# Kernel tuning notes

Measured on AMD Instinct MI355X. Metric: run time of the kernel, lower is better.

## Reference

```python
import jax, jax.numpy as jnp
import numpy as np

K = 3
OFFSET_SCALE = 0.25
GN_GROUPS = 8
GN_EPS = 1e-5


def setup_inputs() -> dict:
    key = jax.random.key(0)
    k1, k2, k3 = jax.random.split(key, 3)
    N, C, H, W = 4, 128, 96, 96
    Cout = 128
    x = jax.random.normal(k1, (N, C, H, W), dtype=jnp.float32)
    # offset head: small random weights so offsets are modest (tanh tames anyway)
    w_head = jax.random.normal(k2, (3, C, 3, 3), dtype=jnp.float32) * 0.05
    b_head = jnp.zeros((3,), dtype=jnp.float32)
    # kaiming-ish scale for the deform conv weight: sqrt(2 / fan_out)
    w_dcn = jax.random.normal(k3, (Cout, C, 3, 3), dtype=jnp.float32) * np.sqrt(2.0 / (Cout * 9))
    gn_gamma = jnp.ones((Cout,), dtype=jnp.float32)
    gn_beta = jnp.zeros((Cout,), dtype=jnp.float32)
    return {"x": x, "w_head": w_head, "b_head": b_head, "w_dcn": w_dcn,
            "gn_gamma": gn_gamma, "gn_beta": gn_beta}


def _conv3x3(x, w, b):
    y = jax.lax.conv_general_dilated(
        x, w, window_strides=(1, 1), padding=((1, 1), (1, 1)),
        dimension_numbers=("NCHW", "OIHW", "NCHW"))
    return y + b[None, :, None, None]


def _deform_sample(xn, py, px):
    # xn: (C,H,W); py/px: (9,H,W) absolute sampling coords (y=row, x=col)
    C, H, W = xn.shape
    y0 = jnp.floor(py).astype(jnp.int32)
    x0 = jnp.floor(px).astype(jnp.int32)
    fy = py - y0
    fx = px - x0
    xf = xn.reshape(C, H * W)

    def corner(yi, xi, wgt):
        valid = (yi >= 0) & (yi < H) & (xi >= 0) & (xi < W)
        idx = jnp.clip(yi, 0, H - 1) * W + jnp.clip(xi, 0, W - 1)  # (9,H,W)
        v = xf[:, idx.reshape(-1)].reshape(C, *idx.shape)  # (C,9,H,W)
        return v * (wgt * valid)[None]

    return (corner(y0, x0, (1 - fy) * (1 - fx))
            + corner(y0, x0 + 1, (1 - fy) * fx)
            + corner(y0 + 1, x0, fy * (1 - fx))
            + corner(y0 + 1, x0 + 1, fy * fx))


def reference(x, w_head, b_head, w_dcn, gn_gamma, gn_beta):
    N, C, H, W = x.shape
    Cout = w_dcn.shape[0]
    stride, pad, dil = 1, 1, 1

    head = _conv3x3(x, w_head, b_head)                 # (N,3,H,W)
    dx, dy, m = head[:, :1], head[:, 1:2], head[:, 2:3]
    mask = jax.nn.sigmoid(m)                           # (N,1,H,W) broadcast over 9 taps
    dx = OFFSET_SCALE * jnp.tanh(dx)
    dy = OFFSET_SCALE * jnp.tanh(dy)

    # serpentine 18-channel offsets, mmcv layout: (oy, ox) pairs per kernel tap
    z = jnp.zeros_like(dx)
    offs = jnp.concatenate(
        [z, z, z, dy, z, -dy, dx, z, z, z, -dx, z, dx, dy, dx, -dy, -dx, dy], axis=1)
    offs = offs.reshape(N, 9, 2, H, W)
    oy, ox = offs[:, :, 0], offs[:, :, 1]              # (N,9,H,W)

    ky = jnp.arange(9) // 3
    kx = jnp.arange(9) % 3
    base_y = (jnp.arange(H) * stride - pad)[None, :, None] + (ky * dil)[:, None, None]
    base_x = (jnp.arange(W) * stride - pad)[None, None, :] + (kx * dil)[:, None, None]
    py = base_y[None] + oy                             # (N,9,H,W)
    px = base_x[None] + ox

    sampled = jax.vmap(_deform_sample)(x, py, px)      # (N,C,9,H,W)
    sampled = sampled * mask[:, None]                  # modulated

    y = jnp.einsum('nckhw,ock->nohw', sampled, w_dcn.reshape(Cout, C, 9))

    # GroupNorm(8, Cout) + ReLU
    G = min(GN_GROUPS, Cout)
    yg = y.reshape(N, G, Cout // G, H, W)
    mu = yg.mean(axis=(2, 3, 4), keepdims=True)
    var = yg.var(axis=(2, 3, 4), keepdims=True)
    yn = ((yg - mu) * jax.lax.rsqrt(var + GN_EPS)).reshape(N, Cout, H, W)
    yn = yn * gn_gamma[None, :, None, None] + gn_beta[None, :, None, None]
    return jax.nn.relu(yn)
```

## Files before the change

### kernel.cpp

```cpp
#include <hip/hip_runtime.h>
#include <hip/hip_bf16.h>
#include <math.h>

#define NB   4
#define CIN  128
#define HH   96
#define WW   96
#define HWN  (HH*WW)
#define NHW  (NB*HWN)
#define COUT 128
#define KW   9
#define KDIM (CIN*KW)
#define GSZ  16
#define PXB  32
#define NBLK (NHW/PXB)

typedef __attribute__((ext_vector_type(8))) short bf16x8;
typedef __attribute__((ext_vector_type(4))) float f32x4;

#define OFF_WAH   0
#define OFF_DX    147456
#define OFF_DY    184320
#define OFF_MASK  221184
#define OFF_GN    258048
#define OFF_MAP   258240
#define OFF_PAIR  258496

#define HEADB 1152

__device__ __forceinline__ ushort f2bf(float f) {
    union { float f; uint u; } v; v.f = f;
    uint r = v.u + 0x7fffu + ((v.u >> 16) & 1u);
    return (ushort)(r >> 16);
}
__device__ __forceinline__ float bf2f(ushort h) {
    union { uint u; float f; } v; v.u = ((uint)h) << 16;
    return v.f;
}

__device__ __forceinline__ void barrier_keep_vm() {
    asm volatile("s_waitcnt lgkmcnt(0)\n\ts_barrier" ::: "memory");
}

__global__ __launch_bounds__(256) void pre_kernel(const float* __restrict__ x,
                                                  const float* __restrict__ w_head,
                                                  const float* __restrict__ b_head,
                                                  const float* __restrict__ wd,
                                                  ushort* __restrict__ wah,
                                                  float* __restrict__ dxv,
                                                  float* __restrict__ dyv,
                                                  float* __restrict__ maskv,
                                                  float* __restrict__ gn_part,
                                                  int* __restrict__ map,
                                                  int* __restrict__ pairB) {
    __shared__ float wl[CIN * 28];
    __shared__ float sp[32][8][13];
    const int b = blockIdx.x, t = threadIdx.x;

    if (b >= HEADB) {
        const int bb = b - HEADB;
        int i = bb * 256 + t;
        {
            int e  = i & 7;
            int l  = (i >> 3) & 63;
            int ot = (i >> 9) & 7;
            int q  = (i >> 12) & 3;
            int k  = i >> 14;
            int o  = ot * 16 + (l & 15);
            int c  = q * 32 + (l >> 4) * 8 + e;
            wah[i] = f2bf(wd[o * KDIM + c * KW + k]);
        }
        if (bb == 0 && t < 128) gn_part[t] = 0.f;
        if (bb == 0 && t < 64) {
            int l = t;
            bf16x8 A1 = {}, B1 = {}, A2 = {}, B2 = {};
            if ((l >> 4) == 0) {
                A1[0] = (short)f2bf((float)((l & 15) + 1));
                B1[0] = (short)f2bf(1.0f);
                A2[0] = (short)f2bf(1.0f);
                B2[0] = (short)f2bf((float)((l & 15) + 1));
            }
            f32x4 d1 = {0.f,0.f,0.f,0.f}, d2 = {0.f,0.f,0.f,0.f};
            d1 = __builtin_amdgcn_mfma_f32_16x16x32_bf16(A1, B1, d1, 0, 0, 0);
            d2 = __builtin_amdgcn_mfma_f32_16x16x32_bf16(A2, B2, d2, 0, 0, 0);
#pragma unroll
            for (int r = 0; r < 4; ++r) {
                int m = (int)(d1[r] + 0.5f) - 1;
                int n = (int)(d2[r] + 0.5f) - 1;
                map[l * 4 + r] = (m << 4) | n;
            }
        }
        if (bb == 1 && t < 64) {
            int l = t;
            union { bf16x8 v; short a[8]; } B;
#pragma unroll
            for (int e = 0; e < 8; ++e) {
                float val = (float)(1u << (((l >> 4) * 8 + e) & 31));
                B.a[e] = (short)f2bf(val);
            }
#pragma unroll
            for (int s = 0; s < 32; ++s) {
                union { bf16x8 v; short a[8]; } A;
#pragma unroll
                for (int e = 0; e < 8; ++e) A.a[e] = 0;
                if ((l >> 4) == (s >> 3)) A.a[s & 7] = (short)f2bf(1.0f);
                f32x4 d = {0.f, 0.f, 0.f, 0.f};
                d = __builtin_amdgcn_mfma_f32_16x16x32_bf16(A.v, B.v, d, 0, 0, 0);
                float v0 = d[0];
                if (l == 0 && v0 > 0.f) {
                    int ex; frexpf(v0, &ex);
                    int j = ex - 1;
                    if (j >= 0 && j < 32) pairB[j] = s;
                }
            }
        }
        return;
    }

    for (int i = t; i < 3456; i += 256) {
        int j = i / KDIM, r = i - j * KDIM;
        int c = r / 9, kk = r - c * 9;
        wl[c * 28 + kk * 3 + j] = w_head[i];
    }
    __syncthreads();

    const int sl = t & 7;
    const int cg = t >> 3;
    const int p0 = b * 32 + sl * 4;
    const int n  = p0 / HWN;
    const int hw = p0 - n * HWN;
    const int h  = hw / WW;
    const int w0 = hw - h * WW;
    const float* xn = x + (size_t)n * CIN * HWN;
    const bool lok = (w0 > 0);
    const bool rok = (w0 < WW - 4);

    float acc[12];
#pragma unroll
    for (int i = 0; i < 12; ++i) acc[i] = 0.f;

#pragma unroll
    for (int cc = 0; cc < 4; ++cc) {
        const int c = cg * 4 + cc;
        const float* xc = xn + (size_t)c * HWN;
        float v[3][6];
#pragma unroll
        for (int r = 0; r < 3; ++r) {
            int y = h - 1 + r;
            if (y >= 0 && y < HH) {
                const float* xr = xc + y * WW + w0;
                float4 m4 = *(const float4*)xr;
                v[r][1] = m4.x; v[r][2] = m4.y; v[r][3] = m4.z; v[r][4] = m4.w;
                v[r][0] = lok ? xr[-1] : 0.f;
                v[r][5] = rok ? xr[4]  : 0.f;
            } else {
#pragma unroll
                for (int i = 0; i < 6; ++i) v[r][i] = 0.f;
            }
        }
        float wr[28];
        const float* wc = &wl[c * 28];
#pragma unroll
        for (int i2 = 0; i2 < 7; ++i2) {
            float4 q4 = *(const float4*)(wc + i2 * 4);
            wr[i2 * 4 + 0] = q4.x; wr[i2 * 4 + 1] = q4.y;
            wr[i2 * 4 + 2] = q4.z; wr[i2 * 4 + 3] = q4.w;
        }
#pragma unroll
        for (int ky = 0; ky < 3; ++ky)
#pragma unroll
            for (int kx = 0; kx < 3; ++kx) {
                const int kk = ky * 3 + kx;
                const float wj0 = wr[kk * 3 + 0];
                const float wj1 = wr[kk * 3 + 1];
                const float wj2 = wr[kk * 3 + 2];
#pragma unroll
                for (int q = 0; q < 4; ++q) {
                    float val = v[ky][q + kx];
                    acc[q * 3 + 0] = fmaf(val, wj0, acc[q * 3 + 0]);
                    acc[q * 3 + 1] = fmaf(val, wj1, acc[q * 3 + 1]);
                    acc[q * 3 + 2] = fmaf(val, wj2, acc[q * 3 + 2]);
                }
            }
    }
#pragma unroll
    for (int i = 0; i < 12; ++i) sp[cg][sl][i] = acc[i];
    __syncthreads();
    if (cg < 8) {
#pragma unroll
        for (int k = 8; k < 32; k += 8)
#pragma unroll
            for (int i = 0; i < 12; ++i) sp[cg][sl][i] += sp[cg + k][sl][i];
    }
    __syncthreads();
    if (t < 32) {
        const int s2 = t >> 2, q = t & 3;
        float b0 = b_head[0], b1 = b_head[1], b2 = b_head[2];
#pragma unroll
        for (int cgi = 0; cgi < 8; ++cgi) {
            b0 += sp[cgi][s2][q * 3 + 0];
            b1 += sp[cgi][s2][q * 3 + 1];
            b2 += sp[cgi][s2][q * 3 + 2];
        }
        int pp = b * 32 + t;
        dxv[pp]   = 0.25f * tanhf(b0);
        dyv[pp]   = 0.25f * tanhf(b1);
        maskv[pp] = 1.f / (1.f + expf(-b2));
    }
}

__global__ __launch_bounds__(256) void dcn_kernel(const float* __restrict__ x,
                                                  const ushort* __restrict__ wah,
                                                  const float* __restrict__ dxv,
                                                  const float* __restrict__ dyv,
                                                  const float* __restrict__ maskv,
                                                  const int* __restrict__ map,
                                                  const int* __restrict__ pairB,
                                                  float* __restrict__ out,
                                                  float* __restrict__ gn_part) {
    __shared__ __attribute__((aligned(16))) ushort sBh[2][4 * PXB * 8];
    __shared__ float sMask[PXB];
    __shared__ float gred[16];

    const int t = threadIdx.x;
    const int lane = t & 63;
    const int wv = t >> 6;
    const int lg = lane >> 4;
    const int ml = lane & 15;
    const int pix = t & 31;
    const int sg  = t >> 5;

    int b = blockIdx.x;
    int nb = (b & 7) * (NBLK / 8) + (b >> 3);
    const int p0  = nb * PXB;
    const int n   = p0 / HWN;
    const int hw0 = p0 % HWN;
    const float* xn = x + (size_t)n * CIN * HWN;

    if (t < PXB) sMask[t] = maskv[p0 + t];
    if (t < 16) gred[t] = 0.f;

    const float dxl = dxv[p0 + pix];
    const float dyl = dyv[p0 + pix];
    const int hme = (hw0 + pix) / WW;
    const int wme = (hw0 + pix) % WW;

    int chn[4];
#pragma unroll
    for (int e = 0; e < 4; ++e) chn[e] = pairB[sg * 4 + e] & 31;

    f32x4 acc[2][2];
#pragma unroll
    for (int i = 0; i < 2; i++)
#pragma unroll
        for (int j = 0; j < 2; j++) acc[i][j] = (f32x4){0.f, 0.f, 0.f, 0.f};

    const int oyc[9] = {0, 0, 0, 1, 0, -1, 1, 1, -1};
    const int oxc[9] = {0, 1, -1, 0, 0, 0, 1, -1, 1};
    const int ncl[9] = {1, 2, 2, 2, 1, 2, 4, 4, 4};

    int aa[4]; float wq[4];
    float raw[4][4];
    bf16x8 An0, An1;

    {
        float py = (float)(hme - 1), px = (float)(wme - 1);
        float fy0 = floorf(py), fx0 = floorf(px);
        int y0 = (int)fy0, x0 = (int)fx0;
        float fy = py - fy0, fx = px - fx0;
#pragma unroll
        for (int j = 0; j < 4; ++j) {
            int yy = y0 + (j >> 1), xx = x0 + (j & 1);
            float wb = ((j >> 1) ? fy : 1.f - fy) * ((j & 1) ? fx : 1.f - fx);
            bool ok = (yy >= 0) && (yy < HH) && (xx >= 0) && (xx < WW);
            aa[j] = min(max(yy, 0), HH - 1) * WW + min(max(xx, 0), WW - 1);
            wq[j] = ok ? wb : 0.f;
        }
#pragma unroll
        for (int e = 0; e < 4; ++e) raw[e][0] = xn[(size_t)chn[e] * HWN + aa[0]];
        const size_t abase = (size_t)(wv * 2) * 512 + lane * 8;
        An0 = *(const bf16x8*)(wah + abase);
        An1 = *(const bf16x8*)(wah + abase + 512);
    }

#pragma unroll
    for (int j = 0; j < 36; ++j) {
        const int k = j >> 2;
        const int NC = ncl[k];
        bf16x8 Ah0 = An0, Ah1 = An1;
        union { short4 v; ushort u[4]; } hv;
#pragma unroll
        for (int e = 0; e < 4; ++e) {
            float s = raw[e][0] * wq[0];
            if (NC >= 2) s += raw[e][1] * wq[1];
            if (NC == 4) s += raw[e][2] * wq[2] + raw[e][3] * wq[3];
            hv.u[e] = f2bf(s);
        }
        const int wbase = ((sg >> 1) * PXB + pix) * 8 + (sg & 1) * 4;
        *(short4*)&sBh[j & 1][wbase] = hv.v;
        if (j < 35) {
            const int jn = j + 1, kn = jn >> 2, qn = jn & 3;
            if (qn == 0) {
                const int ky = kn / 3, kx = kn - ky * 3;
                float py = (float)(hme - 1 + ky) + (float)oyc[kn] * dxl;
                float px = (float)(wme - 1 + kx) + (float)oxc[kn] * dyl;
                float fy0 = floorf(py), fx0 = floorf(px);
                int y0 = (int)fy0, x0 = (int)fx0;
                float fy = py - fy0, fx = px - fx0;
#pragma unroll
                for (int jj = 0; jj < 4; ++jj) {
                    int yy = y0 + (jj >> 1), xx = x0 + (jj & 1);
                    float wb = ((jj >> 1) ? fy : 1.f - fy) * ((jj & 1) ? fx : 1.f - fx);
                    bool ok = (yy >= 0) && (yy < HH) && (xx >= 0) && (xx < WW);
                    aa[jj] = min(max(yy, 0), HH - 1) * WW + min(max(xx, 0), WW - 1);
                    wq[jj] = ok ? wb : 0.f;
                }
                if (ncl[kn] == 2 && oxc[kn] == 0) { aa[1] = aa[2]; wq[1] = wq[2]; }
            }
            const int NCn = ncl[kn];
            const int ccn = qn * 32;
#pragma unroll
            for (int e = 0; e < 4; ++e) {
                const float* xc = xn + (size_t)(ccn + chn[e]) * HWN;
                raw[e][0] = xc[aa[0]];
                if (NCn >= 2) raw[e][1] = xc[aa[1]];
                if (NCn == 4) { raw[e][2] = xc[aa[2]]; raw[e][3] = xc[aa[3]]; }
            }
            const size_t abase = (size_t)((kn * 4 + qn) * 8 + wv * 2) * 512 + lane * 8;
            An0 = *(const bf16x8*)(wah + abase);
            An1 = *(const bf16x8*)(wah + abase + 512);
        }
        barrier_keep_vm();
#pragma unroll
        for (int pt = 0; pt < 2; ++pt) {
            const int rbase = (lg * PXB + pt * 16 + ml) * 8;
            bf16x8 Bh = *(const bf16x8*)&sBh[j & 1][rbase];
            acc[0][pt] = __builtin_amdgcn_mfma_f32_16x16x32_bf16(Ah0, Bh, acc[0][pt], 0, 0, 0);
            acc[1][pt] = __builtin_amdgcn_mfma_f32_16x16x32_bf16(Ah1, Bh, acc[1][pt], 0, 0, 0);
        }
    }

    int4 mn4 = *(const int4*)&map[lane * 4];
    int mn[4] = {mn4.x, mn4.y, mn4.z, mn4.w};
    float s1g[2] = {0.f, 0.f}, s2g[2] = {0.f, 0.f};
#pragma unroll
    for (int ot = 0; ot < 2; ++ot) {
        int otile = wv * 32 + ot * 16;
#pragma unroll
        for (int pt = 0; pt < 2; ++pt) {
#pragma unroll
            for (int r = 0; r < 4; ++r) {
                int m = mn[r] >> 4, nn2 = mn[r] & 15;
                int p = pt * 16 + nn2;
                float v = acc[ot][pt][r] * sMask[p];
                s1g[ot] += v;
                s2g[ot] += v * v;
                out[((size_t)n * COUT + otile + m) * HWN + hw0 + p] = v;
            }
        }
    }
#pragma unroll
    for (int ot = 0; ot < 2; ++ot) {
        int g = wv * 2 + ot;
        atomicAdd(&gred[g * 2 + 0], s1g[ot]);
        atomicAdd(&gred[g * 2 + 1], s2g[ot]);
    }
    __syncthreads();
    if (t < 8) {
        atomicAdd(&gn_part[n * 8 + t],      gred[t * 2 + 0]);
        atomicAdd(&gn_part[64 + n * 8 + t], gred[t * 2 + 1]);
    }
}

__global__ __launch_bounds__(256) void gn_apply(float* __restrict__ out,
                                                const float* __restrict__ gn_part,
                                                const float* __restrict__ gamma,
                                                const float* __restrict__ beta) {
    int i4 = blockIdx.x * 256 + threadIdx.x;
    size_t e = (size_t)i4 * 4;
    int og = (int)(e / HWN);
    int n = og >> 7, o = og & 127;
    int s = n * 8 + (o >> 4);
    const float cnt = (float)GSZ * (float)HWN;
    float s1 = gn_part[s], s2 = gn_part[64 + s];
    float mu = s1 / cnt;
    float var = s2 / cnt - mu * mu;
    float inv = rsqrtf(var + 1e-5f);
    float ga = gamma[o] * inv;
    float be = beta[o] - mu * ga;
    float4 v = *(float4*)(out + e);
    v.x = fmaxf(fmaf(v.x, ga, be), 0.f);
    v.y = fmaxf(fmaf(v.y, ga, be), 0.f);
    v.z = fmaxf(fmaf(v.z, ga, be), 0.f);
    v.w = fmaxf(fmaf(v.w, ga, be), 0.f);
    *(float4*)(out + e) = v;
}

extern "C" void kernel_launch(void* const* d_in, const int* in_sizes, int n_in,
                              void* d_out, int out_size, void* d_ws, size_t ws_size,
                              hipStream_t stream) {
    const float* x       = (const float*)d_in[0];
    const float* w_head  = (const float*)d_in[1];
    const float* b_head  = (const float*)d_in[2];
    const float* w_dcn   = (const float*)d_in[3];
    const float* gamma   = (const float*)d_in[4];
    const float* beta    = (const float*)d_in[5];
    float* out = (float*)d_out;
    float* ws  = (float*)d_ws;

    ushort* wah    = (ushort*)(ws + OFF_WAH);
    float* dxv     = ws + OFF_DX;
    float* dyv     = ws + OFF_DY;
    float* maskv   = ws + OFF_MASK;
    float* gn_part = ws + OFF_GN;
    int*   map     = (int*)(ws + OFF_MAP);
    int*   pairB   = (int*)(ws + OFF_PAIR);

    pre_kernel<<<HEADB + 576, 256, 0, stream>>>(x, w_head, b_head, w_dcn, wah,
                                                dxv, dyv, maskv, gn_part, map, pairB);
    dcn_kernel<<<NBLK, 256, 0, stream>>>(x, wah, dxv, dyv, maskv, map, pairB, out, gn_part);
    gn_apply<<<(NB * COUT * HWN) / 4 / 256, 256, 0, stream>>>(out, gn_part, gamma, beta);
}
```

Before: 196.1 us.

## Transpose input to channel-last with permuted channels for vectorized gathers

Adds a transpose kernel that writes x in NHWC layout with channels permuted to match the MFMA pair ordering, so each deformable-sample gather reads four contiguous channels as one float4 instead of four strided scalar loads. This is meant to cut the number of uncoalesced gather transactions in the main DCN kernel. In exchange it adds an extra pass over the full input tensor, a workspace buffer and an extra launch.

Result: no change. 194.3 us (-0.9%).

```diff
diff --git a/kernel.cpp b/kernel.cpp
--- a/kernel.cpp
+++ b/kernel.cpp
@@ -14,6 +14,7 @@
 #define GSZ  16
 #define PXB  32
 #define NBLK (NHW/PXB)
+#define XPB  64
 
 typedef __attribute__((ext_vector_type(8))) short bf16x8;
 typedef __attribute__((ext_vector_type(4))) float f32x4;
@@ -25,6 +26,7 @@
 #define OFF_GN    258048
 #define OFF_MAP   258240
 #define OFF_PAIR  258496
+#define OFF_XT    258560
 
 #define HEADB 1152
 
@@ -32,10 +34,6 @@
     union { float f; uint u; } v; v.f = f;
     uint r = v.u + 0x7fffu + ((v.u >> 16) & 1u);
     return (ushort)(r >> 16);
-}
-__device__ __forceinline__ float bf2f(ushort h) {
-    union { uint u; float f; } v; v.u = ((uint)h) << 16;
-    return v.f;
 }
 
 __device__ __forceinline__ void barrier_keep_vm() {
@@ -209,13 +207,55 @@
     }
 }
 
-__global__ __launch_bounds__(256) void dcn_kernel(const float* __restrict__ x,
+__global__ __launch_bounds__(256) void xpose_kernel(const float* __restrict__ x,
+                                                    const int* __restrict__ pairB,
+                                                    float* __restrict__ xt) {
+    __shared__ float tile[CIN][XPB + 1];
+    __shared__ int sperm[CIN];
+    const int b = blockIdx.x, t = threadIdx.x;
+    const int p0 = b * XPB;
+    const int n  = p0 / HWN, hw0 = p0 % HWN;
+    const float* xn = x + (size_t)n * CIN * HWN + hw0;
+
+    if (t < CIN) {
+        int q = t >> 5, j = t & 31;
+        sperm[t] = q * 32 + (pairB[j] & 31);
+    }
+    __syncthreads();
+
+#pragma unroll
+    for (int rep = 0; rep < 4; ++rep) {
+        const int c  = rep * 32 + (t >> 3);
+        const int px = (t & 7) * 8;
+        const float* src = xn + (size_t)c * HWN + px;
+        float4 a = *(const float4*)src;
+        float4 bq = *(const float4*)(src + 4);
+        tile[c][px + 0] = a.x;  tile[c][px + 1] = a.y;
+        tile[c][px + 2] = a.z;  tile[c][px + 3] = a.w;
+        tile[c][px + 4] = bq.x; tile[c][px + 5] = bq.y;
+        tile[c][px + 6] = bq.z; tile[c][px + 7] = bq.w;
+    }
+    __syncthreads();
+
+    const int px = t >> 2, jg = t & 3;
+    float* dst = xt + ((size_t)p0 + px) * CIN + jg * 32;
+#pragma unroll
+    for (int jj = 0; jj < 32; jj += 4) {
+        float4 v;
+        v.x = tile[sperm[jg * 32 + jj + 0]][px];
+        v.y = tile[sperm[jg * 32 + jj + 1]][px];
+        v.z = tile[sperm[jg * 32 + jj + 2]][px];
+        v.w = tile[sperm[jg * 32 + jj + 3]][px];
+        *(float4*)(dst + jj) = v;
+    }
+}
+
+__global__ __launch_bounds__(256) void dcn_kernel(const float* __restrict__ xt,
                                                   const ushort* __restrict__ wah,
                                                   const float* __restrict__ dxv,
                                                   const float* __restrict__ dyv,
                                                   const float* __restrict__ maskv,
                                                   const int* __restrict__ map,
-                                                  const int* __restrict__ pairB,
                                                   float* __restrict__ out,
                                                   float* __restrict__ gn_part) {
     __shared__ __attribute__((aligned(16))) ushort sBh[2][4 * PXB * 8];
@@ -235,7 +275,7 @@
     const int p0  = nb * PXB;
     const int n   = p0 / HWN;
     const int hw0 = p0 % HWN;
-    const float* xn = x + (size_t)n * CIN * HWN;
+    const float* xtn = xt + (size_t)n * HWN * CIN;
 
     if (t < PXB) sMask[t] = maskv[p0 + t];
     if (t < 16) gred[t] = 0.f;
@@ -245,10 +285,6 @@
     const int hme = (hw0 + pix) / WW;
     const int wme = (hw0 + pix) % WW;
 
-    int chn[4];
-#pragma unroll
-    for (int e = 0; e < 4; ++e) chn[e] = pairB[sg * 4 + e] & 31;
-
     f32x4 acc[2][2];
 #pragma unroll
     for (int i = 0; i < 2; i++)
@@ -260,7 +296,7 @@
     const int ncl[9] = {1, 2, 2, 2, 1, 2, 4, 4, 4};
 
     int aa[4]; float wq[4];
-    float raw[4][4];
+    float4 vr0, vr1, vr2, vr3;
     bf16x8 An0, An1;
 
     {
@@ -276,8 +312,7 @@
             aa[j] = min(max(yy, 0), HH - 1) * WW + min(max(xx, 0), WW - 1);
             wq[j] = ok ? wb : 0.f;
         }
-#pragma unroll
-        for (int e = 0; e < 4; ++e) raw[e][0] = xn[(size_t)chn[e] * HWN + aa[0]];
+        vr0 = *(const float4*)(xtn + ((aa[0] << 7) + sg * 4));
         const size_t abase = (size_t)(wv * 2) * 512 + lane * 8;
         An0 = *(const bf16x8*)(wah + abase);
         An1 = *(const bf16x8*)(wah + abase + 512);
@@ -289,12 +324,21 @@
         const int NC = ncl[k];
         bf16x8 Ah0 = An0, Ah1 = An1;
         union { short4 v; ushort u[4]; } hv;
-#pragma unroll
-        for (int e = 0; e < 4; ++e) {
-            float s = raw[e][0] * wq[0];
-            if (NC >= 2) s += raw[e][1] * wq[1];
-            if (NC == 4) s += raw[e][2] * wq[2] + raw[e][3] * wq[3];
-            hv.u[e] = f2bf(s);
+        {
+            float s0 = vr0.x * wq[0], s1 = vr0.y * wq[0];
+            float s2 = vr0.z * wq[0], s3 = vr0.w * wq[0];
+            if (NC >= 2) {
+                s0 = fmaf(vr1.x, wq[1], s0); s1 = fmaf(vr1.y, wq[1], s1);
+                s2 = fmaf(vr1.z, wq[1], s2); s3 = fmaf(vr1.w, wq[1], s3);
+            }
+            if (NC == 4) {
+                s0 = fmaf(vr2.x, wq[2], s0); s1 = fmaf(vr2.y, wq[2], s1);
+                s2 = fmaf(vr2.z, wq[2], s2); s3 = fmaf(vr2.w, wq[2], s3);
+                s0 = fmaf(vr3.x, wq[3], s0); s1 = fmaf(vr3.y, wq[3], s1);
+                s2 = fmaf(vr3.z, wq[3], s2); s3 = fmaf(vr3.w, wq[3], s3);
+            }
+            hv.u[0] = f2bf(s0); hv.u[1] = f2bf(s1);
+            hv.u[2] = f2bf(s2); hv.u[3] = f2bf(s3);
         }
         const int wbase = ((sg >> 1) * PXB + pix) * 8 + (sg & 1) * 4;
         *(short4*)&sBh[j & 1][wbase] = hv.v;
@@ -318,13 +362,12 @@
                 if (ncl[kn] == 2 && oxc[kn] == 0) { aa[1] = aa[2]; wq[1] = wq[2]; }
             }
             const int NCn = ncl[kn];
-            const int ccn = qn * 32;
-#pragma unroll
-            for (int e = 0; e < 4; ++e) {
-                const float* xc = xn + (size_t)(ccn + chn[e]) * HWN;
-                raw[e][0] = xc[aa[0]];
-                if (NCn >= 2) raw[e][1] = xc[aa[1]];
-                if (NCn == 4) { raw[e][2] = xc[aa[2]]; raw[e][3] = xc[aa[3]]; }
+            const int co = qn * 32 + sg * 4;
+            vr0 = *(const float4*)(xtn + ((aa[0] << 7) + co));
+            if (NCn >= 2) vr1 = *(const float4*)(xtn + ((aa[1] << 7) + co));
+            if (NCn == 4) {
+                vr2 = *(const float4*)(xtn + ((aa[2] << 7) + co));
+                vr3 = *(const float4*)(xtn + ((aa[3] << 7) + co));
             }
             const size_t abase = (size_t)((kn * 4 + qn) * 8 + wv * 2) * 512 + lane * 8;
             An0 = *(const bf16x8*)(wah + abase);
@@ -415,9 +458,11 @@
     float* gn_part = ws + OFF_GN;
     int*   map     = (int*)(ws + OFF_MAP);
     int*   pairB   = (int*)(ws + OFF_PAIR);
+    float* xt      = ws + OFF_XT;
 
     pre_kernel<<<HEADB + 576, 256, 0, stream>>>(x, w_head, b_head, w_dcn, wah,
                                                 dxv, dyv, maskv, gn_part, map, pairB);
-    dcn_kernel<<<NBLK, 256, 0, stream>>>(x, wah, dxv, dyv, maskv, map, pairB, out, gn_part);
+    xpose_kernel<<<NHW / XPB, 256, 0, stream>>>(x, pairB, xt);
+    dcn_kernel<<<NBLK, 256, 0, stream>>>(xt, wah, dxv, dyv, maskv, map, out, gn_part);
     gn_apply<<<(NB * COUT * HWN) / 4 / 256, 256, 0, stream>>>(out, gn_part, gamma, beta);
 }
```
